# Kernel tuning notes

Measured on AMD Instinct MI355X. Metric: run time of the kernel, lower is better.

## Reference

```python
import jax, jax.numpy as jnp
import numpy as np

B, T, K, F, H, LH, OUT = 256, 90, 17, 2, 64, 512, 57
N_PER = T * K  # 1530 nodes per graph
IN1 = K * (H + F)  # 1122
CONNS = [[15,13],[13,11],[16,14],[14,12],[11,12],[5,11],[6,12],[5,6],[5,7],[6,8],[7,9],[8,10],[1,2],[0,1],[0,2],[1,3],[2,4],[3,5],[4,6]]

def _build_edge_index():
    temporal = np.array([[i, i + K] for i in range(N_PER - K)], dtype=np.int64).T
    structural = np.array([[a + i * K, b + i * K] for a, b in CONNS for i in range(T)], dtype=np.int64).T
    e = np.concatenate([temporal, structural], axis=1)
    e = np.concatenate([e, e[::-1]], axis=1)  # bidirectional
    e = np.concatenate([e + g * N_PER for g in range(B)], axis=1)  # batch offsets
    return jnp.asarray(e)


def setup_inputs() -> dict:
    key = jax.random.key(0)
    ks = jax.random.split(key, 40)
    def n(i, shape, s=0.05):
        return jax.random.normal(ks[i], shape, dtype=jnp.float32) * s
    inp = {
        'x': jax.random.normal(ks[0], (B * N_PER, F), dtype=jnp.float32),
        'edge_index': _build_edge_index(),
        'gat1_W': n(1, (F, H), 0.3), 'gat1_asrc': n(2, (H,), 0.3), 'gat1_adst': n(3, (H,), 0.3), 'gat1_b': n(4, (H,)),
        'bn1_g': jnp.ones((H,), jnp.float32), 'bn1_b': jnp.zeros((H,), jnp.float32),
        'gat2_W': n(5, (H, H), 0.1), 'gat2_asrc': n(6, (H,), 0.3), 'gat2_adst': n(7, (H,), 0.3), 'gat2_b': n(8, (H,)),
        'bn2_g': jnp.ones((H,), jnp.float32), 'bn2_b': jnp.zeros((H,), jnp.float32),
        'l1f_wih': n(9, (4 * LH, IN1)), 'l1f_whh': n(10, (4 * LH, LH)), 'l1f_bih': n(11, (4 * LH,)), 'l1f_bhh': n(12, (4 * LH,)),
        'l1b_wih': n(13, (4 * LH, IN1)), 'l1b_whh': n(14, (4 * LH, LH)), 'l1b_bih': n(15, (4 * LH,)), 'l1b_bhh': n(16, (4 * LH,)),
        'l2f_wih': n(17, (4 * LH, 2 * LH)), 'l2f_whh': n(18, (4 * LH, LH)), 'l2f_bih': n(19, (4 * LH,)), 'l2f_bhh': n(20, (4 * LH,)),
        'l2b_wih': n(21, (4 * LH, 2 * LH)), 'l2b_whh': n(22, (4 * LH, LH)), 'l2b_bih': n(23, (4 * LH,)), 'l2b_bhh': n(24, (4 * LH,)),
        'h1_w': n(25, (2 * LH, 256)), 'h1_b': n(26, (256,)),
        'h2_w': n(27, (256, OUT)), 'h2_b': n(28, (OUT,)),
    }
    return inp


def _gat(x, src, dst, W, a_src, a_dst, b):
    # PyG GATConv, heads=1, self-loops included in src/dst
    N = x.shape[0]
    xp = x @ W  # [N, H]
    e = jax.nn.leaky_relu((xp @ a_src)[src] + (xp @ a_dst)[dst], 0.2)  # [E]
    m = jax.ops.segment_max(e, dst, num_segments=N)
    w = jnp.exp(e - m[dst])
    den = jax.ops.segment_sum(w, dst, num_segments=N)
    alpha = w / den[dst]
    out = jax.ops.segment_sum(xp[src] * alpha[:, None], dst, num_segments=N)
    return out + b


def _bn(x, g, b):
    mu = x.mean(0)
    var = ((x - mu) ** 2).mean(0)
    return g * (x - mu) * jax.lax.rsqrt(var + 1e-5) + b


def _lstm_dir(x, wih, whh, bih, bhh):
    Bn, Hh = x.shape[0], whh.shape[1]
    def step(carry, xt):
        h, c = carry
        z = xt @ wih.T + h @ whh.T + bih + bhh
        i, f, g, o = jnp.split(z, 4, axis=-1)  # torch gate order
        c = jax.nn.sigmoid(f) * c + jax.nn.sigmoid(i) * jnp.tanh(g)
        h = jax.nn.sigmoid(o) * jnp.tanh(c)
        return (h, c), h
    h0 = jnp.zeros((Bn, Hh), x.dtype)
    _, hs = jax.lax.scan(step, (h0, h0), jnp.swapaxes(x, 0, 1))
    return jnp.swapaxes(hs, 0, 1)


def _bilstm(x, wf_ih, wf_hh, bf_ih, bf_hh, wb_ih, wb_hh, bb_ih, bb_hh):
    fwd = _lstm_dir(x, wf_ih, wf_hh, bf_ih, bf_hh)
    bwd = _lstm_dir(x[:, ::-1], wb_ih, wb_hh, bb_ih, bb_hh)[:, ::-1]
    return jnp.concatenate([fwd, bwd], axis=-1)


def reference(x, edge_index,
              gat1_W, gat1_asrc, gat1_adst, gat1_b, bn1_g, bn1_b,
              gat2_W, gat2_asrc, gat2_adst, gat2_b, bn2_g, bn2_b,
              l1f_wih, l1f_whh, l1f_bih, l1f_bhh, l1b_wih, l1b_whh, l1b_bih, l1b_bhh,
              l2f_wih, l2f_whh, l2f_bih, l2f_bhh, l2b_wih, l2b_whh, l2b_bih, l2b_bhh,
              h1_w, h1_b, h2_w, h2_b):
    N = x.shape[0]
    sl = jnp.arange(N)
    src = jnp.concatenate([edge_index[0], sl])  # add self loops (GATConv default)
    dst = jnp.concatenate([edge_index[1], sl])
    h = jax.nn.relu(_bn(_gat(x, src, dst, gat1_W, gat1_asrc, gat1_adst, gat1_b), bn1_g, bn1_b))
    h = jax.nn.relu(_bn(_gat(h, src, dst, gat2_W, gat2_asrc, gat2_adst, gat2_b), bn2_g, bn2_b))
    feats = jnp.concatenate([h, x], axis=1).reshape(B, T, IN1)  # [B, 90, 1122]
    o = _bilstm(feats, l1f_wih, l1f_whh, l1f_bih, l1f_bhh, l1b_wih, l1b_whh, l1b_bih, l1b_bhh)
    o = _bilstm(o, l2f_wih, l2f_whh, l2f_bih, l2f_bhh, l2b_wih, l2b_whh, l2b_bih, l2b_bhh)
    o = jax.nn.relu(o @ h1_w + h1_b) @ h2_w + h2_b  # [B, 90, 57]
    return o
```

## Files before the change

### kernel.cpp

```cpp
#include <hip/hip_runtime.h>
#include <cstdint>
#include <cstddef>

#define B_    256
#define T_    90
#define K_    17
#define NPER  1530
#define NN    (B_*NPER)
#define H_    64
#define LH    512
#define G4    2048
#define G8    4096
#define IN1   1122
#define IN1P  1152
#define SEQR  (B_*T_)
#define OUT_  57

typedef unsigned short u16;
typedef __attribute__((ext_vector_type(8))) short short8;
typedef __attribute__((ext_vector_type(4))) float f32x4;

__device__ __forceinline__ float b2f(u16 u){ union{unsigned i; float f;} x; x.i=((unsigned)u)<<16; return x.f; }
__device__ __forceinline__ u16 f2b(float f){ union{float f; unsigned i;} x; x.f=f; unsigned r=x.i+0x7fffu+((x.i>>16)&1u); return (u16)(r>>16); }
__device__ __forceinline__ float sigm(float v){ return 1.f/(1.f+__expf(-v)); }
__device__ __forceinline__ float tanh_(float v){ return 2.f*sigm(2.f*v)-1.f; }

__global__ __launch_bounds__(256)
void stg_sentinel(float* __restrict__ out, int n){
  int i=blockIdx.x*256+threadIdx.x;
  if(i<n) out[i]=123.0f;
}

__global__ __launch_bounds__(256)
void stg_permute_w(const float* __restrict__ src, u16* __restrict__ dst, int Ks, int Kd){
  size_t idx=(size_t)blockIdx.x*256+threadIdx.x;
  int rn=(int)(idx/Kd), kk=(int)(idx%Kd);
  int j=rn>>2, G=rn&3, ro=G*LH+j;
  dst[idx] = (kk<Ks)? f2b(src[(size_t)ro*Ks+kk]) : (u16)0;
}

__global__ __launch_bounds__(256)
void stg_prep_bias(const float* __restrict__ bih, const float* __restrict__ bhh, float* __restrict__ dst){
  int rn=blockIdx.x*256+threadIdx.x;
  int j=rn>>2, G=rn&3, ro=G*LH+j;
  dst[rn]=bih[ro]+bhh[ro];
}

__global__ __launch_bounds__(256)
void stg_transpose_pad(const float* __restrict__ src, u16* __restrict__ dst, int R, int C, int Crows){
  size_t idx=(size_t)blockIdx.x*256+threadIdx.x;
  int c=(int)(idx/R), r=(int)(idx%R);
  dst[idx] = (c<C)? f2b(src[(size_t)r*C+c]) : (u16)0;
  (void)Crows;
}

__global__ __launch_bounds__(256)
void stg_gat1_xp(const float* __restrict__ x, const float* __restrict__ W, u16* __restrict__ xp,
                 const float* __restrict__ as, const float* __restrict__ ad,
                 float* __restrict__ ssrc, float* __restrict__ sdst){
  size_t idx=(size_t)blockIdx.x*256+threadIdx.x;
  size_t n=idx>>6; int c=idx&63;
  float v=x[n*2]*W[c]+x[n*2+1]*W[64+c];
  u16 vb16=f2b(v);
  xp[idx]=vb16;
  float vb=b2f(vb16);
  float s1=vb*as[c], s2=vb*ad[c];
  #pragma unroll
  for(int m=1;m<64;m<<=1){ s1+=__shfl_xor(s1,m); s2+=__shfl_xor(s2,m); }
  if(c==0){ ssrc[n]=s1; sdst[n]=s2; }
}

__global__ __launch_bounds__(256)
void stg_scores(const u16* __restrict__ xp, const float* __restrict__ as, const float* __restrict__ ad,
                float* __restrict__ ssrc, float* __restrict__ sdst){
  const int lane=threadIdx.x&63;
  const size_t n=(size_t)blockIdx.x*4+(threadIdx.x>>6);
  float v=b2f(xp[n*64+lane]);
  float s1=v*as[lane], s2=v*ad[lane];
  #pragma unroll
  for(int m=1;m<64;m<<=1){ s1+=__shfl_xor(s1,m); s2+=__shfl_xor(s2,m); }
  if(lane==0){ ssrc[n]=s1; sdst[n]=s2; }
}

__constant__ int c_deg[17]={2,3,3,2,2,4,4,2,2,1,1,3,3,2,2,1,1};
__constant__ int c_adj[17][4]={{1,2,0,0},{2,0,3,0},{1,0,4,0},{1,5,0,0},{2,6,0,0},
 {11,6,7,3},{12,5,8,4},{5,9,0,0},{6,10,0,0},{7,0,0,0},{8,0,0,0},
 {13,12,5,0},{14,11,6,0},{15,11,0,0},{16,12,0,0},{13,0,0,0},{14,0,0,0}};

__global__ __launch_bounds__(256)
void stg_gat_agg(const u16* __restrict__ xp, const float* __restrict__ ssrc, const float* __restrict__ sdst,
                 const float* __restrict__ bias, u16* __restrict__ out){
  const int lane=threadIdx.x&63;
  const int n=blockIdx.x*4+(threadIdx.x>>6);
  const int r=n%NPER, t=r/K_, k=r%K_;
  const int dg=c_deg[k];
  const int base=n-k;
  const int nb0=n;
  const int nb1=(t>0)?      n-K_ : n;  const bool v1=(t>0);
  const int nb2=(t<T_-1)?   n+K_ : n;  const bool v2=(t<T_-1);
  const int nb3=base+c_adj[k][0];
  const int nb4=base+c_adj[k][1];      const bool v4=(dg>1);
  const int nb5=base+c_adj[k][2];      const bool v5=(dg>2);
  const int nb6=base+c_adj[k][3];      const bool v6=(dg>3);
  const float sd=sdst[n];
  const float NEG=-1e30f;
  auto lrelu=[](float v){ return v>0.f? v : 0.2f*v; };
  float e0=lrelu(ssrc[nb0]+sd);
  float e1=v1? lrelu(ssrc[nb1]+sd) : NEG;
  float e2=v2? lrelu(ssrc[nb2]+sd) : NEG;
  float e3=    lrelu(ssrc[nb3]+sd);
  float e4=v4? lrelu(ssrc[nb4]+sd) : NEG;
  float e5=v5? lrelu(ssrc[nb5]+sd) : NEG;
  float e6=v6? lrelu(ssrc[nb6]+sd) : NEG;
  float mx=fmaxf(fmaxf(fmaxf(e0,e1),fmaxf(e2,e3)),fmaxf(fmaxf(e4,e5),e6));
  float w0=__expf(e0-mx), w1=__expf(e1-mx), w2=__expf(e2-mx), w3=__expf(e3-mx);
  float w4=__expf(e4-mx), w5=__expf(e5-mx), w6=__expf(e6-mx);
  const float inv=1.f/(w0+w1+w2+w3+w4+w5+w6);
  float acc = w0*b2f(xp[(size_t)nb0*64+lane])
            + w1*b2f(xp[(size_t)nb1*64+lane])
            + w2*b2f(xp[(size_t)nb2*64+lane])
            + w3*b2f(xp[(size_t)nb3*64+lane])
            + w4*b2f(xp[(size_t)nb4*64+lane])
            + w5*b2f(xp[(size_t)nb5*64+lane])
            + w6*b2f(xp[(size_t)nb6*64+lane]);
  out[(size_t)n*64+lane]=f2b(acc*inv+bias[lane]);
}

__global__ __launch_bounds__(256)
void stg_bn_part(const u16* __restrict__ in, float* __restrict__ part){
  const int c=threadIdx.x&63, sub=threadIdx.x>>6;
  float s=0.f,q=0.f;
  for(size_t n=(size_t)blockIdx.x*4+sub; n<NN; n+=1024){
    float v=b2f(in[n*64+c]); s+=v; q+=v*v;
  }
  __shared__ float sS[4][64], sQ[4][64];
  sS[sub][c]=s; sQ[sub][c]=q;
  __syncthreads();
  if(sub==0){
    float a=0,bq=0;
    for(int i=0;i<4;i++){a+=sS[i][c]; bq+=sQ[i][c];}
    part[blockIdx.x*128+c*2]=a; part[blockIdx.x*128+c*2+1]=bq;
  }
}

__global__ void stg_bn_fin(const float* __restrict__ part, const float* __restrict__ g,
                           const float* __restrict__ b, float* __restrict__ stats){
  const int c=threadIdx.x;
  float s=0,q=0;
  for(int p=0;p<256;++p){ s+=part[p*128+c*2]; q+=part[p*128+c*2+1]; }
  const float invN=1.f/(float)NN;
  float mu=s*invN, var=q*invN-mu*mu;
  float istd=rsqrtf(var+1e-5f);
  float a=g[c]*istd;
  stats[c*2]=a; stats[c*2+1]=b[c]-mu*a;
}

__global__ __launch_bounds__(256)
void stg_bn_apply(const u16* __restrict__ in, const float* __restrict__ stats, u16* __restrict__ out){
  size_t idx=(size_t)blockIdx.x*256+threadIdx.x;
  int c=idx&63;
  float v=b2f(in[idx])*stats[c*2]+stats[c*2+1];
  out[idx]=f2b(fmaxf(v,0.f));
}

__global__ __launch_bounds__(256)
void stg_build_feats(const u16* __restrict__ h2, const float* __restrict__ x, u16* __restrict__ feats){
  size_t idx=(size_t)blockIdx.x*256+threadIdx.x;
  size_t row=idx/IN1P; int cc=(int)(idx%IN1P);
  u16 outv=0;
  if(cc<IN1){
    int k=cc/66, f=cc%66;
    size_t g=row/T_, t=row%T_;
    size_t node=g*NPER+t*K_+k;
    outv = (f<64)? h2[node*64+f] : f2b(x[node*2+(f-64)]);
  }
  feats[idx]=outv;
}

template<int BM,int BN,int WR,int WC,int EPI>
__global__ __launch_bounds__(WR*WC*64)
void stg_gemm_bt(const u16* __restrict__ A, int ldA,
                 const u16* __restrict__ Bt, int ldB,
                 void* __restrict__ Cp, int ldC, int K,
                 const float* __restrict__ bias)
{
  constexpr int THREADS=WR*WC*64;
  constexpr int WM=BM/WR, WN=BN/WC, FM=WM/16, FN=WN/16;
  constexpr int QA=BM*4/THREADS, QB=BN*4/THREADS;
  __shared__ u16 As[2][BM*32];
  __shared__ u16 Bs[2][BN*32];
  const int tid=threadIdx.x, w=tid>>6, lane=tid&63;
  const int wr=w/WC, wc=w%WC;
  const size_t row0=(size_t)blockIdx.y*BM;
  const size_t col0=(size_t)blockIdx.x*BN;
  f32x4 acc[FM][FN];
  #pragma unroll
  for(int i=0;i<FM;i++)
    #pragma unroll
    for(int j=0;j<FN;j++)
      #pragma unroll
      for(int r=0;r<4;r++) acc[i][j][r]=0.f;

  const u16* gA[QA]; const u16* gB[QB]; int lA_[QA], lB_[QB];
  #pragma unroll
  for(int q=0;q<QA;++q){
    const int s=tid+q*THREADS;
    gA[q]=A+(row0+(s>>2))*(size_t)ldA+(s&3)*8;
    lA_[q]=s*8;
  }
  #pragma unroll
  for(int q=0;q<QB;++q){
    const int s=tid+q*THREADS;
    gB[q]=Bt+(col0+(s>>2))*(size_t)ldB+(s&3)*8;
    lB_[q]=s*8;
  }

  short8 ra[QA], rb[QB];
  #pragma unroll
  for(int q=0;q<QA;++q) ra[q]=*(const short8*)(gA[q]);
  #pragma unroll
  for(int q=0;q<QB;++q) rb[q]=*(const short8*)(gB[q]);
  #pragma unroll
  for(int q=0;q<QA;++q) *(short8*)&As[0][lA_[q]]=ra[q];
  #pragma unroll
  for(int q=0;q<QB;++q) *(short8*)&Bs[0][lB_[q]]=rb[q];

  const int nIter=K/32;
  int cur=0;
  for(int it=0; it<nIter; ++it){
    if(it<nIter-1){
      #pragma unroll
      for(int q=0;q<QA;++q) ra[q]=*(const short8*)(gA[q]+(it+1)*32);
      #pragma unroll
      for(int q=0;q<QB;++q) rb[q]=*(const short8*)(gB[q]+(it+1)*32);
    }
    __syncthreads();
    short8 af[FM], bf[FN];
    #pragma unroll
    for(int mi=0;mi<FM;mi++)
      af[mi]=*(const short8*)&As[cur][(wr*WM+mi*16+(lane&15))*32+(lane>>4)*8];
    #pragma unroll
    for(int ni=0;ni<FN;ni++)
      bf[ni]=*(const short8*)&Bs[cur][(wc*WN+ni*16+(lane&15))*32+(lane>>4)*8];
    #pragma unroll
    for(int mi=0;mi<FM;mi++)
      #pragma unroll
      for(int ni=0;ni<FN;ni++)
        acc[mi][ni]=__builtin_amdgcn_mfma_f32_16x16x32_bf16(af[mi],bf[ni],acc[mi][ni],0,0,0);
    if(it<nIter-1){
      #pragma unroll
      for(int q=0;q<QA;++q) *(short8*)&As[cur^1][lA_[q]]=ra[q];
      #pragma unroll
      for(int q=0;q<QB;++q) *(short8*)&Bs[cur^1][lB_[q]]=rb[q];
    }
    cur^=1;
  }
  #pragma unroll
  for(int mi=0;mi<FM;mi++)
   #pragma unroll
   for(int ni=0;ni<FN;ni++)
    #pragma unroll
    for(int r=0;r<4;r++){
      const size_t row=row0+wr*WM+mi*16+(lane>>4)*4+r;
      const size_t col=col0+wc*WN+ni*16+(lane&15);
      float v=acc[mi][ni][r];
      if constexpr (EPI==0){ ((u16*)Cp)[row*ldC+col]=f2b(v); }
      else if constexpr (EPI==1){ v+=bias[col]; ((u16*)Cp)[row*ldC+col]=f2b(fmaxf(v,0.f)); }
      else { if(col<OUT_){ ((float*)Cp)[row*ldC+col]=v+bias[col]; } }
    }
}

__global__ __launch_bounds__(512)
void stg_lstm_step(const u16* __restrict__ hprev, u16* __restrict__ hcur,
                   float* __restrict__ cst,
                   const u16* __restrict__ whh,
                   const u16* __restrict__ xprAll,
                   const float* __restrict__ bias,
                   u16* __restrict__ seq,
                   int t)
{
  __shared__ u16 As[2][2*2048];
  __shared__ u16 Bs[2][2*2048];
  __shared__ float Zs[64*64];
  const int dir = blockIdx.z;
  const int tt  = dir ? (T_-1-t) : t;
  const u16* xp = xprAll + (size_t)dir*G4;
  const u16* Ap = hprev + (size_t)dir*B_*LH;
  const u16* Bp = whh   + (size_t)dir*G4*LH;
  const int tid=threadIdx.x, w=tid>>6, lane=tid&63;
  const int wr=w>>2, wc=w&3;
  const int row0=blockIdx.x*64, col0=blockIdx.y*64;

  const int gc_ = col0 + wc*16 + (lane&15);
  const float bias_v = bias[dir*G4 + gc_];
  u16 xpr_[2][4];
  #pragma unroll
  for(int mi=0;mi<2;mi++)
    #pragma unroll
    for(int r=0;r<4;r++){
      const int b=row0+wr*32+mi*16+(lane>>4)*4+r;
      xpr_[mi][r]=xp[(size_t)(b*T_+tt)*G8+gc_];
    }
  const int rlA=tid>>4,        uA=tid&15;
  const int rlB=(tid+512)>>4,  uB=tid&15;
  const size_t ciA=(size_t)dir*B_*LH + (size_t)(row0+rlA)*LH + (col0>>2)+uA;
  const size_t ciB=(size_t)dir*B_*LH + (size_t)(row0+rlB)*LH + (col0>>2)+uB;
  const float cprevA=cst[ciA];
  const float cprevB=cst[ciB];

  const int sp=w>>2, ss=w&3;
  const int srow=ss*16+(lane>>2);
  const int scO=(lane&3)*8;
  const u16* gA = Ap + (size_t)(row0+srow)*LH + sp*32 + scO;
  const u16* gB = Bp + (size_t)(col0+srow)*LH + sp*32 + scO;
  const int lA = sp*2048 + srow*32 + scO;

  f32x4 acc[2];
  #pragma unroll
  for(int i=0;i<2;i++)
    #pragma unroll
    for(int r=0;r<4;r++) acc[i][r]=0.f;

  short8 ra=*(const short8*)(gA);
  short8 rb=*(const short8*)(gB);
  *(short8*)&As[0][lA]=ra; *(short8*)&Bs[0][lA]=rb;

  int cur=0;
  for(int it=0; it<8; ++it){
    if(it<7){ ra=*(const short8*)(gA+(it+1)*64); rb=*(const short8*)(gB+(it+1)*64); }
    __syncthreads();
    #pragma unroll
    for(int p=0;p<2;++p){
      short8 af[2], bf;
      #pragma unroll
      for(int mi=0;mi<2;mi++)
        af[mi]=*(const short8*)&As[cur][p*2048+(wr*32+mi*16+(lane&15))*32+(lane>>4)*8];
      bf=*(const short8*)&Bs[cur][p*2048+(wc*16+(lane&15))*32+(lane>>4)*8];
      #pragma unroll
      for(int mi=0;mi<2;mi++)
        acc[mi]=__builtin_amdgcn_mfma_f32_16x16x32_bf16(af[mi],bf,acc[mi],0,0,0);
    }
    if(it<7){ *(short8*)&As[cur^1][lA]=ra; *(short8*)&Bs[cur^1][lA]=rb; }
    cur^=1;
  }
  #pragma unroll
  for(int mi=0;mi<2;mi++)
    #pragma unroll
    for(int r=0;r<4;r++){
      const int rl=wr*32+mi*16+(lane>>4)*4+r;
      const int cl=wc*16+(lane&15);
      Zs[rl*64+cl]=acc[mi][r] + b2f(xpr_[mi][r]) + bias_v;
    }
  __syncthreads();
  {
    const float zi=Zs[rlA*64+4*uA+0], zf=Zs[rlA*64+4*uA+1];
    const float zg=Zs[rlA*64+4*uA+2], zo=Zs[rlA*64+4*uA+3];
    float c = sigm(zf)*cprevA + sigm(zi)*tanh_(zg);
    cst[ciA]=c;
    float h = sigm(zo)*tanh_(c);
    hcur[ciA]=f2b(h);
    seq[(size_t)((row0+rlA)*T_+tt)*(2*LH) + (size_t)dir*LH + (col0>>2)+uA]=f2b(h);
  }
  {
    const float zi=Zs[rlB*64+4*uB+0], zf=Zs[rlB*64+4*uB+1];
    const float zg=Zs[rlB*64+4*uB+2], zo=Zs[rlB*64+4*uB+3];
    float c = sigm(zf)*cprevB + sigm(zi)*tanh_(zg);
    cst[ciB]=c;
    float h = sigm(zo)*tanh_(c);
    hcur[ciB]=f2b(h);
    seq[(size_t)((row0+rlB)*T_+tt)*(2*LH) + (size_t)dir*LH + (col0>>2)+uB]=f2b(h);
  }
}

extern "C" void kernel_launch(void* const* d_in, const int* in_sizes, int n_in,
                              void* d_out, int out_size, void* d_ws, size_t ws_size,
                              hipStream_t stream)
{
  (void)in_sizes; (void)n_in;
  const float* x    =(const float*)d_in[0];
  const float* g1W  =(const float*)d_in[2];
  const float* g1as =(const float*)d_in[3];
  const float* g1ad =(const float*)d_in[4];
  const float* g1b  =(const float*)d_in[5];
  const float* bn1g =(const float*)d_in[6];
  const float* bn1b =(const float*)d_in[7];
  const float* g2W  =(const float*)d_in[8];
  const float* g2as =(const float*)d_in[9];
  const float* g2ad =(const float*)d_in[10];
  const float* g2b  =(const float*)d_in[11];
  const float* bn2g =(const float*)d_in[12];
  const float* bn2b =(const float*)d_in[13];
  const float* l1f_wih=(const float*)d_in[14];
  const float* l1f_whh=(const float*)d_in[15];
  const float* l1f_bih=(const float*)d_in[16];
  const float* l1f_bhh=(const float*)d_in[17];
  const float* l1b_wih=(const float*)d_in[18];
  const float* l1b_whh=(const float*)d_in[19];
  const float* l1b_bih=(const float*)d_in[20];
  const float* l1b_bhh=(const float*)d_in[21];
  const float* l2f_wih=(const float*)d_in[22];
  const float* l2f_whh=(const float*)d_in[23];
  const float* l2f_bih=(const float*)d_in[24];
  const float* l2f_bhh=(const float*)d_in[25];
  const float* l2b_wih=(const float*)d_in[26];
  const float* l2b_whh=(const float*)d_in[27];
  const float* l2b_bih=(const float*)d_in[28];
  const float* l2b_bhh=(const float*)d_in[29];
  const float* h1w  =(const float*)d_in[30];
  const float* h1b  =(const float*)d_in[31];
  const float* h2w  =(const float*)d_in[32];
  const float* h2b  =(const float*)d_in[33];

  const size_t SZ_w1ih  = (size_t)G4*IN1P*2;
  const size_t SZ_w2ih  = (size_t)G4*1024*2;
  const size_t SZ_whh   = (size_t)4*G4*LH*2;
  const size_t SZ_bias  = (size_t)4*G4*4;
  const size_t SZ_w2gT  = (size_t)64*64*2;
  const size_t SZ_h1T   = (size_t)256*1024*2;
  const size_t SZ_h2T   = (size_t)64*256*2;
  const size_t SZ_part  = (size_t)256*128*4;
  const size_t SZ_stats = (size_t)64*2*4;
  const size_t SZ_hs    = (size_t)2*B_*LH*2;
  const size_t SZ_cs    = (size_t)2*B_*LH*4;
  const size_t SZ_xprA  = (size_t)SEQR*G8*2;
  const size_t SZ_feats = (size_t)SEQR*IN1P*2;
  const size_t SZ_gat   = (size_t)NN*64*2;
  const size_t SZ_sc    = (size_t)NN*4;

  char* base=(char*)d_ws; size_t o=0;
  auto take=[&](size_t b)->size_t{ size_t r=o; o=(o+b+255)&~(size_t)255; return r; };
  const size_t off_w1ih = take(2*SZ_w1ih);
  const size_t off_whh  = take(SZ_whh);
  const size_t off_bias = take(SZ_bias);
  const size_t off_w2gT = take(SZ_w2gT);
  const size_t off_h1T  = take(SZ_h1T);
  const size_t off_h2T  = take(SZ_h2T);
  const size_t off_part = take(SZ_part);
  const size_t off_stat = take(SZ_stats);
  const size_t off_hs0  = take(SZ_hs);
  const size_t off_hs1  = take(SZ_hs);
  const size_t off_cs   = take(SZ_cs);
  const size_t off_R12  = take(SZ_xprA);
  const size_t off_R3   = take(SZ_feats);
  const size_t NEED = o;
  if (NEED > ws_size) {
    stg_sentinel<<<(out_size+255)/256,256,0,stream>>>((float*)d_out, out_size);
    return;
  }

  u16* w1ihF=(u16*)(base+off_w1ih);
  u16* w1ihB=(u16*)(base+off_w1ih+SZ_w1ih);
  u16* w2ihF=(u16*)(base+off_w1ih);
  u16* w2ihB=(u16*)(base+off_w1ih+SZ_w2ih);
  u16* whhAll=(u16*)(base+off_whh);
  float* biasAll=(float*)(base+off_bias);
  u16* w2gT=(u16*)(base+off_w2gT);
  u16* h1T =(u16*)(base+off_h1T);
  u16* h2T =(u16*)(base+off_h2T);
  float* part=(float*)(base+off_part);
  float* stats=(float*)(base+off_stat);
  u16* hs0=(u16*)(base+off_hs0);
  u16* hs1=(u16*)(base+off_hs1);
  float* cs=(float*)(base+off_cs);
  u16* xprAll=(u16*)(base+off_R12);
  u16* xpB_=(u16*)(base+off_R12);
  u16* aggB=(u16*)(base+off_R12+SZ_gat);
  u16* hB  =(u16*)(base+off_R12+2*SZ_gat);
  float* ssrc=(float*)(base+off_R12+3*SZ_gat);
  float* sdst=(float*)(base+off_R12+3*SZ_gat+SZ_sc);
  u16* mid =(u16*)(base+off_R12);
  u16* feats=(u16*)(base+off_R3);
  u16* seq  =(u16*)(base+off_R3);

  stg_permute_w<<<G4*IN1P/256,256,0,stream>>>(l1f_wih,w1ihF,IN1,IN1P);
  stg_permute_w<<<G4*IN1P/256,256,0,stream>>>(l1b_wih,w1ihB,IN1,IN1P);
  stg_permute_w<<<G4*LH/256,256,0,stream>>>(l1f_whh,whhAll+0*(size_t)G4*LH,LH,LH);
  stg_permute_w<<<G4*LH/256,256,0,stream>>>(l1b_whh,whhAll+1*(size_t)G4*LH,LH,LH);
  stg_permute_w<<<G4*LH/256,256,0,stream>>>(l2f_whh,whhAll+2*(size_t)G4*LH,LH,LH);
  stg_permute_w<<<G4*LH/256,256,0,stream>>>(l2b_whh,whhAll+3*(size_t)G4*LH,LH,LH);
  stg_prep_bias<<<G4/256,256,0,stream>>>(l1f_bih,l1f_bhh,biasAll+0*G4);
  stg_prep_bias<<<G4/256,256,0,stream>>>(l1b_bih,l1b_bhh,biasAll+1*G4);
  stg_prep_bias<<<G4/256,256,0,stream>>>(l2f_bih,l2f_bhh,biasAll+2*G4);
  stg_prep_bias<<<G4/256,256,0,stream>>>(l2b_bih,l2b_bhh,biasAll+3*G4);
  stg_transpose_pad<<<64*64/256,256,0,stream>>>(g2W,w2gT,64,64,64);
  stg_transpose_pad<<<256*1024/256,256,0,stream>>>(h1w,h1T,1024,256,256);
  stg_transpose_pad<<<64*256/256,256,0,stream>>>(h2w,h2T,256,57,64);

  stg_gat1_xp<<<NN*64/256,256,0,stream>>>(x,g1W,xpB_,g1as,g1ad,ssrc,sdst);
  stg_gat_agg<<<NN/4,256,0,stream>>>(xpB_,ssrc,sdst,g1b,aggB);
  stg_bn_part<<<256,256,0,stream>>>(aggB,part);
  stg_bn_fin<<<1,64,0,stream>>>(part,bn1g,bn1b,stats);
  stg_bn_apply<<<NN*64/256,256,0,stream>>>(aggB,stats,hB);

  stg_gemm_bt<128,64,2,2,0><<<dim3(1,NN/128),256,0,stream>>>(hB,64,w2gT,64,xpB_,64,64,nullptr);
  stg_scores<<<NN/4,256,0,stream>>>(xpB_,g2as,g2ad,ssrc,sdst);
  stg_gat_agg<<<NN/4,256,0,stream>>>(xpB_,ssrc,sdst,g2b,aggB);
  stg_bn_part<<<256,256,0,stream>>>(aggB,part);
  stg_bn_fin<<<1,64,0,stream>>>(part,bn2g,bn2b,stats);
  stg_bn_apply<<<NN*64/256,256,0,stream>>>(aggB,stats,hB);

  stg_build_feats<<<SEQR*IN1P/256,256,0,stream>>>(hB,x,feats);

  stg_gemm_bt<128,256,2,4,0><<<dim3(G8/256,SEQR/128),512,0,stream>>>(feats,IN1P,w1ihF,IN1P,xprAll,G8,IN1P,nullptr);
  stg_permute_w<<<G4*1024/256,256,0,stream>>>(l2f_wih,w2ihF,1024,1024);
  stg_permute_w<<<G4*1024/256,256,0,stream>>>(l2b_wih,w2ihB,1024,1024);

  hipMemsetAsync(hs0,0,SZ_hs,stream);
  hipMemsetAsync(cs,0,SZ_cs,stream);
  for(int t=0;t<T_;++t){
    u16* hp=(t&1)?hs1:hs0; u16* hc=(t&1)?hs0:hs1;
    stg_lstm_step<<<dim3(B_/64,G4/64,2),512,0,stream>>>(hp,hc,cs,whhAll,xprAll,biasAll,seq,t);
  }

  stg_gemm_bt<128,256,2,4,0><<<dim3(G8/256,SEQR/128),512,0,stream>>>(seq,1024,w2ihF,1024,xprAll,G8,1024,nullptr);
  hipMemsetAsync(hs0,0,SZ_hs,stream);
  hipMemsetAsync(cs,0,SZ_cs,stream);
  for(int t=0;t<T_;++t){
    u16* hp=(t&1)?hs1:hs0; u16* hc=(t&1)?hs0:hs1;
    stg_lstm_step<<<dim3(B_/64,G4/64,2),512,0,stream>>>(hp,hc,cs,whhAll+(size_t)2*G4*LH,xprAll,biasAll+2*G4,seq,t);
  }

  stg_gemm_bt<128,128,2,2,1><<<dim3(256/128,SEQR/128),256,0,stream>>>(seq,1024,h1T,1024,mid,256,1024,h1b);
  stg_gemm_bt<128,64,2,2,2><<<dim3(1,SEQR/128),256,0,stream>>>(mid,256,h2T,256,d_out,OUT_,256,h2b);
}
```

Measured before the change: 2.341 ms.

## Triple-buffer GEMM shared memory with two-deep register prefetch

Restructures the bf16 MFMA GEMM main loop to use three LDS stages and two register staging sets. Global loads are issued two K-tiles ahead and each LDS write follows the MFMA compute, leaving one barrier per K-step. This hides more global-memory latency behind compute, at the cost of extra LDS and registers, which may lower occupancy.

New measurement: 2.525 ms. 7.9% more time.

```diff
diff --git a/kernel.cpp b/kernel.cpp
--- a/kernel.cpp
+++ b/kernel.cpp
@@ -187,8 +187,8 @@
   constexpr int THREADS=WR*WC*64;
   constexpr int WM=BM/WR, WN=BN/WC, FM=WM/16, FN=WN/16;
   constexpr int QA=BM*4/THREADS, QB=BN*4/THREADS;
-  __shared__ u16 As[2][BM*32];
-  __shared__ u16 Bs[2][BN*32];
+  __shared__ u16 As[3][BM*32];
+  __shared__ u16 Bs[3][BN*32];
   const int tid=threadIdx.x, w=tid>>6, lane=tid&63;
   const int wr=w/WC, wc=w%WC;
   const size_t row0=(size_t)blockIdx.y*BM;
@@ -215,46 +215,77 @@
     lB_[q]=s*8;
   }
 
-  short8 ra[QA], rb[QB];
-  #pragma unroll
-  for(int q=0;q<QA;++q) ra[q]=*(const short8*)(gA[q]);
-  #pragma unroll
-  for(int q=0;q<QB;++q) rb[q]=*(const short8*)(gB[q]);
-  #pragma unroll
-  for(int q=0;q<QA;++q) *(short8*)&As[0][lA_[q]]=ra[q];
-  #pragma unroll
-  for(int q=0;q<QB;++q) *(short8*)&Bs[0][lB_[q]]=rb[q];
-
-  const int nIter=K/32;
-  int cur=0;
-  for(int it=0; it<nIter; ++it){
-    if(it<nIter-1){
-      #pragma unroll
-      for(int q=0;q<QA;++q) ra[q]=*(const short8*)(gA[q]+(it+1)*32);
-      #pragma unroll
-      for(int q=0;q<QB;++q) rb[q]=*(const short8*)(gB[q]+(it+1)*32);
-    }
-    __syncthreads();
+  auto COMPUTE=[&](int buf){
     short8 af[FM], bf[FN];
     #pragma unroll
     for(int mi=0;mi<FM;mi++)
-      af[mi]=*(const short8*)&As[cur][(wr*WM+mi*16+(lane&15))*32+(lane>>4)*8];
+      af[mi]=*(const short8*)&As[buf][(wr*WM+mi*16+(lane&15))*32+(lane>>4)*8];
     #pragma unroll
     for(int ni=0;ni<FN;ni++)
-      bf[ni]=*(const short8*)&Bs[cur][(wc*WN+ni*16+(lane&15))*32+(lane>>4)*8];
+      bf[ni]=*(const short8*)&Bs[buf][(wc*WN+ni*16+(lane&15))*32+(lane>>4)*8];
     #pragma unroll
     for(int mi=0;mi<FM;mi++)
       #pragma unroll
       for(int ni=0;ni<FN;ni++)
         acc[mi][ni]=__builtin_amdgcn_mfma_f32_16x16x32_bf16(af[mi],bf[ni],acc[mi][ni],0,0,0);
-    if(it<nIter-1){
-      #pragma unroll
-      for(int q=0;q<QA;++q) *(short8*)&As[cur^1][lA_[q]]=ra[q];
-      #pragma unroll
-      for(int q=0;q<QB;++q) *(short8*)&Bs[cur^1][lB_[q]]=rb[q];
-    }
-    cur^=1;
-  }
+  };
+
+  short8 raA[QA], rbA[QB], raB[QA], rbB[QB];
+  const int nIter=K/32;
+
+  #pragma unroll
+  for(int q=0;q<QA;++q) raA[q]=*(const short8*)(gA[q]);
+  #pragma unroll
+  for(int q=0;q<QB;++q) rbA[q]=*(const short8*)(gB[q]);
+  #pragma unroll
+  for(int q=0;q<QA;++q) *(short8*)&As[0][lA_[q]]=raA[q];
+  #pragma unroll
+  for(int q=0;q<QB;++q) *(short8*)&Bs[0][lB_[q]]=rbA[q];
+  if(nIter>1){
+    #pragma unroll
+    for(int q=0;q<QA;++q) raB[q]=*(const short8*)(gA[q]+32);
+    #pragma unroll
+    for(int q=0;q<QB;++q) rbB[q]=*(const short8*)(gB[q]+32);
+  }
+  __syncthreads();
+
+  int cur=0;
+  for(int it=0; it<nIter; it+=2){
+    if(it+2<nIter){
+      #pragma unroll
+      for(int q=0;q<QA;++q) raA[q]=*(const short8*)(gA[q]+(it+2)*32);
+      #pragma unroll
+      for(int q=0;q<QB;++q) rbA[q]=*(const short8*)(gB[q]+(it+2)*32);
+    }
+    COMPUTE(cur);
+    const int b1=(cur+1)%3;
+    if(it+1<nIter){
+      #pragma unroll
+      for(int q=0;q<QA;++q) *(short8*)&As[b1][lA_[q]]=raB[q];
+      #pragma unroll
+      for(int q=0;q<QB;++q) *(short8*)&Bs[b1][lB_[q]]=rbB[q];
+    }
+    __syncthreads();
+    if(it+1<nIter){
+      if(it+3<nIter){
+        #pragma unroll
+        for(int q=0;q<QA;++q) raB[q]=*(const short8*)(gA[q]+(it+3)*32);
+        #pragma unroll
+        for(int q=0;q<QB;++q) rbB[q]=*(const short8*)(gB[q]+(it+3)*32);
+      }
+      COMPUTE(b1);
+      const int b2=(cur+2)%3;
+      if(it+2<nIter){
+        #pragma unroll
+        for(int q=0;q<QA;++q) *(short8*)&As[b2][lA_[q]]=raA[q];
+        #pragma unroll
+        for(int q=0;q<QB;++q) *(short8*)&Bs[b2][lB_[q]]=rbA[q];
+      }
+      __syncthreads();
+    }
+    cur=(cur+2)%3;
+  }
+
   #pragma unroll
   for(int mi=0;mi<FM;mi++)
    #pragma unroll
```
